# Performance work log

Hardware: AMD Instinct MI355X
Metric: run time of the kernel (lower is better)

Reference implementation:

```python
import jax, jax.numpy as jnp
import numpy as np

S, E, D, L, K = 32, 64, 256, 5, 5  # sentences, entities, feat dim, labels, support shots


def setup_inputs() -> dict:
    key = jax.random.key(0)
    k1, k2, k3, k4, k5, k6, k7 = jax.random.split(key, 7)
    scale = 1.0 / np.sqrt(D)
    return {
        "sup_entities": jax.random.normal(k1, (L, K, 2 * D), jnp.float32),
        "sup_context": jax.random.normal(k2, (L, K, D), jnp.float32),
        "x": jax.random.normal(k3, (S, E, D), jnp.float32),
        "context": jax.random.normal(k4, (S, E, E, D), jnp.float32),
        "W": jax.random.normal(k5, (D, D), jnp.float32) * scale,
        "Wself": jax.random.normal(k6, (D, D), jnp.float32) * scale,
        "counts": jax.random.randint(k7, (L,), 0, 9, jnp.int32),
    }


def reference(sup_entities, sup_context, x, context, W, Wself, counts):
    # per-label instance-count bias c_n = |n| / (total - |n|)
    cnt = counts.astype(jnp.float32) + 1.0
    total = jnp.sum(cnt)
    c = cnt / (total - cnt)  # [L]

    # prototypes (mean over support instances)
    proto = jnp.mean(sup_entities, axis=1)      # [L, 2D]
    ctx_center = jnp.mean(sup_context, axis=1)  # [L, D]

    # per-label edge weights: 1 / ||context[s,u,v] - ctx_center[k]||^2
    cn2 = jnp.sum(context * context, axis=-1)                        # [S,E,E]
    cc2 = jnp.sum(ctx_center * ctx_center, axis=-1)                  # [L]
    cross = jnp.einsum('suvd,kd->suvk', context, ctx_center)         # [S,E,E,L]
    d2 = cn2[..., None] - 2.0 * cross + cc2                          # [S,E,E,L]
    diag = jnp.eye(E, dtype=bool)
    w = jnp.where(diag[None, :, :, None], 0.0, 1.0 / jnp.maximum(d2, 1e-8))

    # GNN propagation per label: out[s,k,v] = x[s,v]@Wself + sum_u w[s,u,v,k] * (x[s,u]@W)
    xW = x @ W        # [S,E,D]
    xself = x @ Wself  # [S,E,D]
    out = xself[:, None, :, :] + jnp.einsum('suvk,sud->skvd', w, xW)  # [S,L,E,D]

    # squared distance of pred = cat(out[j], out[jp]) to each prototype n
    pa, pb = proto[:, :D], proto[:, D:]  # [L,D] each

    def sqd(o, p):  # o:[S,L,E,D], p:[L,D] -> [S,L,E,L]
        return (jnp.sum(o * o, axis=-1)[..., None]
                - 2.0 * jnp.einsum('skvd,nd->skvn', o, p)
                + jnp.sum(p * p, axis=-1))

    da = sqd(out, pa)  # [S,L,E,L]
    db = sqd(out, pb)  # [S,L,E,L]
    logits = da[:, :, :, None, :] + db[:, :, None, :, :] + c  # [S,L,E,E,L]
    pred = jax.nn.softmax(logits, axis=-1)
    # -> [sentence, entity_j, entity_j', weight_label_k, class_n]
    return jnp.transpose(pred, (0, 2, 3, 1, 4))
```

## Files before the change

### kernel.cpp

```cpp
#include <hip/hip_runtime.h>
#include <hip/hip_bf16.h>

#define SS 32
#define EE 64
#define DD 256
#define LL 5

typedef unsigned int uint32;

static __device__ __forceinline__ ushort f2bf(float f) {
    uint32 u = __float_as_uint(f);
    uint32 r = (u + 0x7FFFu + ((u >> 16) & 1u)) >> 16;
    return (ushort)r;
}
static __device__ __forceinline__ float bf2f(ushort h) {
    return __uint_as_float(((uint32)h) << 16);
}

template <int CTRL>
static __device__ __forceinline__ float dpp_add(float x) {
    int y = __builtin_amdgcn_update_dpp(0, __float_as_int(x), CTRL, 0xF, 0xF, true);
    return x + __int_as_float(y);
}
static __device__ __forceinline__ float red16(float x) {
    x = dpp_add<0xB1>(x);
    x = dpp_add<0x4E>(x);
    x = dpp_add<0x141>(x);
    x = dpp_add<0x140>(x);
    return x;
}


__global__ __launch_bounds__(256) void k0_setup(
    const float* __restrict__ sup_entities,
    const float* __restrict__ sup_context,
    const int*   __restrict__ counts,
    float* __restrict__ ws) {
    int b = blockIdx.x;
    int t = threadIdx.x, lane = t & 63, wv = t >> 6;
    __shared__ float part[4];

    if (b < 10) {
        int k = (b >= 5) ? b - 5 : b;
        int off = (b >= 5) ? 256 : 0;
        float s = 0.f;
#pragma unroll
        for (int j = 0; j < 5; j++) s += sup_entities[(k * 5 + j) * 512 + off + t];
        float m = s * 0.2f;
        ws[(b >= 5 ? 1280 : 0) + k * 256 + t] = m;
        float p = m * m;
#pragma unroll
        for (int o = 1; o < 64; o <<= 1) p += __shfl_xor(p, o);
        if (lane == 0) part[wv] = p;
        __syncthreads();
        if (t == 0) ws[2560 + b] = part[0] + part[1] + part[2] + part[3];
    } else {
        int k = b - 10;
        float s = 0.f;
#pragma unroll
        for (int j = 0; j < 5; j++) s += sup_context[(k * 5 + j) * DD + t];
        float m = s * 0.2f;
        ws[2576 + k * 256 + t] = m;
        float p = m * m;
#pragma unroll
        for (int o = 1; o < 64; o <<= 1) p += __shfl_xor(p, o);
        if (lane == 0) part[wv] = p;
        __syncthreads();
        if (t == 0) ws[3856 + k] = part[0] + part[1] + part[2] + part[3];
        if (b == 10 && t == 1) {
            float cnt[5], tot = 0.f;
#pragma unroll
            for (int q = 0; q < 5; q++) { cnt[q] = (float)counts[q] + 1.0f; tot += cnt[q]; }
#pragma unroll
            for (int q = 0; q < 5; q++) ws[2570 + q] = cnt[q] / (tot - cnt[q]);
        }
    }
}

__global__ __attribute__((amdgpu_waves_per_eu(2, 2))) __launch_bounds__(256)
void k1_gemm(
    const float* __restrict__ x, const float* __restrict__ W,
    const float* __restrict__ Wself, float* __restrict__ ws) {
    float* xself = ws + 4096;
    ushort* xw = (ushort*)(ws + 528384);

    int row0 = blockIdx.x * 8;
    int t = threadIdx.x, lane = t & 63, wv = t >> 6;

    float xreg[8];
    const float* xbase = x + row0 * DD + wv * 64 + lane;
#pragma unroll
    for (int r = 0; r < 8; r++) xreg[r] = xbase[r * DD];

    float4 accW[8], accS[8];
#pragma unroll
    for (int r = 0; r < 8; r++) {
        accW[r] = make_float4(0.f, 0.f, 0.f, 0.f);
        accS[r] = make_float4(0.f, 0.f, 0.f, 0.f);
    }
    const float4* Wp  = ((const float4*)W) + lane;
    const float4* Wsp = ((const float4*)Wself) + lane;
#pragma unroll 2
    for (int i = 0; i < 64; i++) {
        int kk = wv * 64 + i;
        float4 w4  = Wp[kk * 64];
        float4 ws4 = Wsp[kk * 64];
#pragma unroll
        for (int r = 0; r < 8; r++) {
            float xs = __uint_as_float(
                (uint32)__builtin_amdgcn_readlane((int)__float_as_uint(xreg[r]), i));
            accW[r].x = fmaf(xs, w4.x, accW[r].x);
            accW[r].y = fmaf(xs, w4.y, accW[r].y);
            accW[r].z = fmaf(xs, w4.z, accW[r].z);
            accW[r].w = fmaf(xs, w4.w, accW[r].w);
            accS[r].x = fmaf(xs, ws4.x, accS[r].x);
            accS[r].y = fmaf(xs, ws4.y, accS[r].y);
            accS[r].z = fmaf(xs, ws4.z, accS[r].z);
            accS[r].w = fmaf(xs, ws4.w, accS[r].w);
        }
    }
    __shared__ float4 redbuf[4][8][64];
#pragma unroll
    for (int r = 0; r < 8; r++) redbuf[wv][r][lane] = accS[r];
    __syncthreads();
    {
        int r = t >> 5;
#pragma unroll
        for (int f = 0; f < 2; f++) {
            int l4 = (t & 31) + 32 * f;
            float4 a = redbuf[0][r][l4], b = redbuf[1][r][l4];
            float4 c = redbuf[2][r][l4], d = redbuf[3][r][l4];
            float4 s4 = make_float4(a.x + b.x + c.x + d.x, a.y + b.y + c.y + d.y,
                                    a.z + b.z + c.z + d.z, a.w + b.w + c.w + d.w);
            *(float4*)&xself[(row0 + r) * DD + l4 * 4] = s4;
        }
    }
    __syncthreads();
#pragma unroll
    for (int r = 0; r < 8; r++) redbuf[wv][r][lane] = accW[r];
    __syncthreads();
    {
        int r = t >> 5;
#pragma unroll
        for (int f = 0; f < 2; f++) {
            int l4 = (t & 31) + 32 * f;
            float4 a = redbuf[0][r][l4], b = redbuf[1][r][l4];
            float4 c = redbuf[2][r][l4], d = redbuf[3][r][l4];
            float4 s4 = make_float4(a.x + b.x + c.x + d.x, a.y + b.y + c.y + d.y,
                                    a.z + b.z + c.z + d.z, a.w + b.w + c.w + d.w);
            ushort4 h;
            h.x = f2bf(s4.x); h.y = f2bf(s4.y); h.z = f2bf(s4.z); h.w = f2bf(s4.w);
            *(ushort4*)&xw[(row0 + r) * DD + l4 * 4] = h;
        }
    }
}

__global__ __attribute__((amdgpu_waves_per_eu(4, 4))) __launch_bounds__(256)
void k2_w(const float* __restrict__ context, float* __restrict__ ws) {
    float* wt = ws + 790528;

    int bx = blockIdx.x;
    int s = bx >> 6, u = bx & 63;
    int t = threadIdx.x, lane = t & 63, wv = t >> 6;
    int g = lane >> 4, gl = lane & 15;
    int G = wv * 4 + g;

    __shared__ float cc_l[1280];
    __shared__ float cc2_l[8];
    __shared__ float wbuf[5][64];

    for (int i = t; i < 320; i += 256)
        ((float4*)cc_l)[i] = ((const float4*)(ws + 2576))[i];
    if (t < 5) cc2_l[t] = ws[3856 + t];
    __syncthreads();

    float4 cc[5][4];
    float cc2r[5];
#pragma unroll
    for (int k = 0; k < 5; k++) {
#pragma unroll
        for (int j = 0; j < 4; j++)
            cc[k][j] = *(const float4*)&cc_l[k * 256 + j * 64 + gl * 4];
        cc2r[k] = cc2_l[k];
    }

    const float* base = context + (size_t)bx * (EE * DD) + gl * 4;
#pragma unroll
    for (int p = 0; p < 4; p++) {
        int v = p * 16 + G;
        const float* row = base + v * DD;
        float4 a[4];
#pragma unroll
        for (int j = 0; j < 4; j++) a[j] = *(const float4*)&row[j * 64];

        float cn = 0.f;
        float cr[5] = {0.f, 0.f, 0.f, 0.f, 0.f};
#pragma unroll
        for (int j = 0; j < 4; j++) {
            float4 c4 = a[j];
            cn = fmaf(c4.x, c4.x, fmaf(c4.y, c4.y, fmaf(c4.z, c4.z, fmaf(c4.w, c4.w, cn))));
#pragma unroll
            for (int k = 0; k < 5; k++) {
                float4 pp = cc[k][j];
                cr[k] = fmaf(c4.x, pp.x, fmaf(c4.y, pp.y, fmaf(c4.z, pp.z, fmaf(c4.w, pp.w, cr[k]))));
            }
        }
        cn = red16(cn);
#pragma unroll
        for (int k = 0; k < 5; k++) cr[k] = red16(cr[k]);
        if (gl == 0) {
#pragma unroll
            for (int k = 0; k < 5; k++) {
                float d2 = cn - 2.f * cr[k] + cc2r[k];
                wbuf[k][v] = (u == v) ? 0.f : 1.f / fmaxf(d2, 1e-8f);
            }
        }
    }
    __syncthreads();
    for (int i = t; i < 320; i += 256) {
        int k = i >> 6, v = i & 63;
        wt[(((size_t)s * 5 + k) * 64 + u) * 64 + v] = wbuf[k][v];
    }
}

__global__ __attribute__((amdgpu_waves_per_eu(2, 2))) __launch_bounds__(256)
void kB(const float* __restrict__ ws) {
    const ushort* xw = (const ushort*)(ws + 528384);
    const float* xself = ws + 4096;
    const float* wt = ws + 790528;
    float* da = (float*)(ws + 1445888);
    float* db = (float*)(ws + 1497088);

    int bx = blockIdx.x;
    int s = bx >> 4, vg = bx & 15;
    int t = threadIdx.x, lane = t & 63, wv = t >> 6;

    __shared__ ushort xw_l[64][256];
    __shared__ float  w_l[5][64][4];

    {
        const uint4* src = (const uint4*)(xw + (size_t)s * (EE * DD));
        uint4* dst = (uint4*)&xw_l[0][0];
#pragma unroll
        for (int j = 0; j < 8; j++) dst[j * 256 + t] = src[j * 256 + t];
    }
    for (int i = t; i < 320; i += 256) {
        int k = i >> 6, u = i & 63;
        *(float4*)&w_l[k][u][0] =
            *(const float4*)&wt[(((size_t)s * 5 + k) * 64 + u) * 64 + vg * 4];
    }
    __syncthreads();

    int v = vg * 4 + wv;
    float4 acc[5];
    {
        float4 xs = *(const float4*)&xself[((size_t)s * 64 + v) * DD + lane * 4];
#pragma unroll
        for (int k = 0; k < 5; k++) acc[k] = xs;
    }

#pragma unroll 4
    for (int u = 0; u < 64; u++) {
        ushort4 h4 = *(const ushort4*)&xw_l[u][lane * 4];
        float4 xv = make_float4(bf2f(h4.x), bf2f(h4.y), bf2f(h4.z), bf2f(h4.w));
#pragma unroll
        for (int k = 0; k < 5; k++) {
            float wk = w_l[k][u][wv];
            acc[k].x = fmaf(wk, xv.x, acc[k].x);
            acc[k].y = fmaf(wk, xv.y, acc[k].y);
            acc[k].z = fmaf(wk, xv.z, acc[k].z);
            acc[k].w = fmaf(wk, xv.w, acc[k].w);
        }
    }

    float4 pA[5], pB[5];
#pragma unroll
    for (int n = 0; n < 5; n++) {
        pA[n] = *(const float4*)&ws[n * 256 + lane * 4];
        pB[n] = *(const float4*)&ws[1280 + n * 256 + lane * 4];
    }
    float pa2r[5], pb2r[5];
#pragma unroll
    for (int n = 0; n < 5; n++) { pa2r[n] = ws[2560 + n]; pb2r[n] = ws[2565 + n]; }

#pragma unroll
    for (int k = 0; k < 5; k++) {
        float4 o = acc[k];
        float r[11];
        r[0] = fmaf(o.x, o.x, fmaf(o.y, o.y, fmaf(o.z, o.z, o.w * o.w)));
#pragma unroll
        for (int n = 0; n < 5; n++) {
            float4 p = pA[n];
            r[1 + n] = fmaf(o.x, p.x, fmaf(o.y, p.y, fmaf(o.z, p.z, o.w * p.w)));
            float4 q = pB[n];
            r[6 + n] = fmaf(o.x, q.x, fmaf(o.y, q.y, fmaf(o.z, q.z, o.w * q.w)));
        }
#pragma unroll
        for (int off = 1; off < 64; off <<= 1) {
#pragma unroll
            for (int q = 0; q < 11; q++) r[q] += __shfl_xor(r[q], off);
        }
        if (lane == 0) {
            size_t idx = (((size_t)s * 5 + k) * 64 + v) * 5;
#pragma unroll
            for (int n = 0; n < 5; n++) {
                da[idx + n] = r[0] - 2.f * r[1 + n] + pa2r[n];
                db[idx + n] = r[0] - 2.f * r[6 + n] + pb2r[n];
            }
        }
    }
}

__global__ __launch_bounds__(320) void kC(const float* __restrict__ ws,
                                          float* __restrict__ out) {
    const float* da = ws + 1445888;
    const float* db = ws + 1497088;
    int bx = blockIdx.x;
    int s = bx >> 6, v1 = bx & 63;
    int t = threadIdx.x;
    int v2 = t / 5, k = t - v2 * 5;

    __shared__ float ob[1600];
    __shared__ float cvs[5];
    if (t < 5) cvs[t] = ws[2570 + t];

    const float* dap = da + (((size_t)s * 5 + k) * 64 + v1) * 5;
    const float* dbp = db + (((size_t)s * 5 + k) * 64 + v2) * 5;
    float l0[5];
#pragma unroll
    for (int n = 0; n < 5; n++) l0[n] = dap[n] + dbp[n];
    __syncthreads();
    float m = -3.4e38f;
#pragma unroll
    for (int n = 0; n < 5; n++) { l0[n] += cvs[n]; m = fmaxf(m, l0[n]); }
    float e[5], sum = 0.f;
#pragma unroll
    for (int n = 0; n < 5; n++) { e[n] = __expf(l0[n] - m); sum += e[n]; }
    float r = 1.f / sum;
#pragma unroll
    for (int n = 0; n < 5; n++) ob[t * 5 + n] = e[n] * r;
    __syncthreads();

    const float4* ob4 = (const float4*)ob;
    float4* op = (float4*)(out + (size_t)bx * 1600);
    for (int i = t; i < 400; i += 320) op[i] = ob4[i];
}

extern "C" void kernel_launch(void* const* d_in, const int* in_sizes, int n_in,
                              void* d_out, int out_size, void* d_ws, size_t ws_size,
                              hipStream_t stream) {
    const float* sup_entities = (const float*)d_in[0];
    const float* sup_context  = (const float*)d_in[1];
    const float* x            = (const float*)d_in[2];
    const float* context      = (const float*)d_in[3];
    const float* W            = (const float*)d_in[4];
    const float* Wself        = (const float*)d_in[5];
    const int*   counts       = (const int*)d_in[6];
    float* out = (float*)d_out;
    float* ws = (float*)d_ws;

    k0_setup<<<15, 256, 0, stream>>>(sup_entities, sup_context, counts, ws);
    k2_w<<<SS * EE, 256, 0, stream>>>(context, ws);
    k1_gemm<<<256, 256, 0, stream>>>(x, W, Wself, ws);
    kB<<<512, 256, 0, stream>>>(ws);
    kC<<<SS * EE, 320, 0, stream>>>(ws, out);
}
```

Measured before the change: 73.09 us.

## Fuse setup into weight kernel and use readlane broadcasts in propagation

Folds the prototype/context-center setup kernel into the edge-weight kernel, so each weight block recomputes the context centers and their norms from the support context, and 10 extra blocks handle the entity prototypes and count bias. This removes one kernel launch and its dependency. In the propagation kernel, edge weights are loaded per lane into registers and broadcast with readlane instead of staged through shared memory, and the loop is fully unrolled. The 64-lane reductions switch from shuffle-xor to DPP row ops plus readlane. The cost is redundant per-block recomputation of the centers and larger unrolled code.

```diff
diff --git a/kernel.cpp b/kernel.cpp
--- a/kernel.cpp
+++ b/kernel.cpp
@@ -29,18 +29,28 @@
     x = dpp_add<0x140>(x);
     return x;
 }
-
-
-__global__ __launch_bounds__(256) void k0_setup(
-    const float* __restrict__ sup_entities,
-    const float* __restrict__ sup_context,
-    const int*   __restrict__ counts,
-    float* __restrict__ ws) {
-    int b = blockIdx.x;
+static __device__ __forceinline__ float red64_scalar(float x) {
+    x = red16(x);
+    x = dpp_add<0x142>(x);
+    x = dpp_add<0x143>(x);
+    return __uint_as_float((uint32)__builtin_amdgcn_readlane(__float_as_int(x), 63));
+}
+
+
+__global__ __attribute__((amdgpu_waves_per_eu(4, 4))) __launch_bounds__(256)
+void k2f(const float* __restrict__ context, const float* __restrict__ sup_context,
+         const float* __restrict__ sup_entities, const int* __restrict__ counts,
+         float* __restrict__ ws) {
+    int bx = blockIdx.x;
     int t = threadIdx.x, lane = t & 63, wv = t >> 6;
+
+    __shared__ float cc_l[1280];
+    __shared__ float cc2_l[8];
+    __shared__ float wbuf[5][64];
     __shared__ float part[4];
 
-    if (b < 10) {
+    if (bx >= 2048) {
+        int b = bx - 2048;
         int k = (b >= 5) ? b - 5 : b;
         int off = (b >= 5) ? 256 : 0;
         float s = 0.f;
@@ -54,26 +64,86 @@
         if (lane == 0) part[wv] = p;
         __syncthreads();
         if (t == 0) ws[2560 + b] = part[0] + part[1] + part[2] + part[3];
-    } else {
-        int k = b - 10;
-        float s = 0.f;
-#pragma unroll
-        for (int j = 0; j < 5; j++) s += sup_context[(k * 5 + j) * DD + t];
-        float m = s * 0.2f;
-        ws[2576 + k * 256 + t] = m;
-        float p = m * m;
-#pragma unroll
-        for (int o = 1; o < 64; o <<= 1) p += __shfl_xor(p, o);
-        if (lane == 0) part[wv] = p;
-        __syncthreads();
-        if (t == 0) ws[3856 + k] = part[0] + part[1] + part[2] + part[3];
-        if (b == 10 && t == 1) {
+        if (b == 0 && t == 1) {
             float cnt[5], tot = 0.f;
 #pragma unroll
             for (int q = 0; q < 5; q++) { cnt[q] = (float)counts[q] + 1.0f; tot += cnt[q]; }
 #pragma unroll
             for (int q = 0; q < 5; q++) ws[2570 + q] = cnt[q] / (tot - cnt[q]);
         }
+        return;
+    }
+
+    int s = bx >> 6, u = bx & 63;
+    int g = lane >> 4, gl = lane & 15;
+    int G = wv * 4 + g;
+
+    for (int i = t; i < 1280; i += 256) {
+        int k = i >> 8, d = i & 255;
+        float sum = 0.f;
+#pragma unroll
+        for (int j = 0; j < 5; j++) sum += sup_context[(k * 5 + j) * DD + d];
+        cc_l[i] = sum * 0.2f;
+    }
+    __syncthreads();
+    if (t < 80) {
+        int k = t >> 4, gg = t & 15;
+        float p = 0.f;
+#pragma unroll
+        for (int j = 0; j < 16; j++) { float v = cc_l[k * 256 + gg * 16 + j]; p = fmaf(v, v, p); }
+#pragma unroll
+        for (int o = 1; o < 16; o <<= 1) p += __shfl_xor(p, o);
+        if (gg == 0) cc2_l[k] = p;
+    }
+    __syncthreads();
+
+    float4 cc[5][4];
+    float cc2r[5];
+#pragma unroll
+    for (int k = 0; k < 5; k++) {
+#pragma unroll
+        for (int j = 0; j < 4; j++)
+            cc[k][j] = *(const float4*)&cc_l[k * 256 + j * 64 + gl * 4];
+        cc2r[k] = cc2_l[k];
+    }
+
+    float* wt = ws + 790528;
+    const float* base = context + (size_t)bx * (EE * DD) + gl * 4;
+#pragma unroll
+    for (int p = 0; p < 4; p++) {
+        int v = p * 16 + G;
+        const float* row = base + v * DD;
+        float4 a[4];
+#pragma unroll
+        for (int j = 0; j < 4; j++) a[j] = *(const float4*)&row[j * 64];
+
+        float cn = 0.f;
+        float cr[5] = {0.f, 0.f, 0.f, 0.f, 0.f};
+#pragma unroll
+        for (int j = 0; j < 4; j++) {
+            float4 c4 = a[j];
+            cn = fmaf(c4.x, c4.x, fmaf(c4.y, c4.y, fmaf(c4.z, c4.z, fmaf(c4.w, c4.w, cn))));
+#pragma unroll
+            for (int k = 0; k < 5; k++) {
+                float4 pp = cc[k][j];
+                cr[k] = fmaf(c4.x, pp.x, fmaf(c4.y, pp.y, fmaf(c4.z, pp.z, fmaf(c4.w, pp.w, cr[k]))));
+            }
+        }
+        cn = red16(cn);
+#pragma unroll
+        for (int k = 0; k < 5; k++) cr[k] = red16(cr[k]);
+        if (gl == 0) {
+#pragma unroll
+            for (int k = 0; k < 5; k++) {
+                float d2 = cn - 2.f * cr[k] + cc2r[k];
+                wbuf[k][v] = (u == v) ? 0.f : 1.f / fmaxf(d2, 1e-8f);
+            }
+        }
+    }
+    __syncthreads();
+    for (int i = t; i < 320; i += 256) {
+        int k = i >> 6, v = i & 63;
+        wt[(((size_t)s * 5 + k) * 64 + u) * 64 + v] = wbuf[k][v];
     }
 }
 
@@ -155,74 +225,6 @@
     }
 }
 
-__global__ __attribute__((amdgpu_waves_per_eu(4, 4))) __launch_bounds__(256)
-void k2_w(const float* __restrict__ context, float* __restrict__ ws) {
-    float* wt = ws + 790528;
-
-    int bx = blockIdx.x;
-    int s = bx >> 6, u = bx & 63;
-    int t = threadIdx.x, lane = t & 63, wv = t >> 6;
-    int g = lane >> 4, gl = lane & 15;
-    int G = wv * 4 + g;
-
-    __shared__ float cc_l[1280];
-    __shared__ float cc2_l[8];
-    __shared__ float wbuf[5][64];
-
-    for (int i = t; i < 320; i += 256)
-        ((float4*)cc_l)[i] = ((const float4*)(ws + 2576))[i];
-    if (t < 5) cc2_l[t] = ws[3856 + t];
-    __syncthreads();
-
-    float4 cc[5][4];
-    float cc2r[5];
-#pragma unroll
-    for (int k = 0; k < 5; k++) {
-#pragma unroll
-        for (int j = 0; j < 4; j++)
-            cc[k][j] = *(const float4*)&cc_l[k * 256 + j * 64 + gl * 4];
-        cc2r[k] = cc2_l[k];
-    }
-
-    const float* base = context + (size_t)bx * (EE * DD) + gl * 4;
-#pragma unroll
-    for (int p = 0; p < 4; p++) {
-        int v = p * 16 + G;
-        const float* row = base + v * DD;
-        float4 a[4];
-#pragma unroll
-        for (int j = 0; j < 4; j++) a[j] = *(const float4*)&row[j * 64];
-
-        float cn = 0.f;
-        float cr[5] = {0.f, 0.f, 0.f, 0.f, 0.f};
-#pragma unroll
-        for (int j = 0; j < 4; j++) {
-            float4 c4 = a[j];
-            cn = fmaf(c4.x, c4.x, fmaf(c4.y, c4.y, fmaf(c4.z, c4.z, fmaf(c4.w, c4.w, cn))));
-#pragma unroll
-            for (int k = 0; k < 5; k++) {
-                float4 pp = cc[k][j];
-                cr[k] = fmaf(c4.x, pp.x, fmaf(c4.y, pp.y, fmaf(c4.z, pp.z, fmaf(c4.w, pp.w, cr[k]))));
-            }
-        }
-        cn = red16(cn);
-#pragma unroll
-        for (int k = 0; k < 5; k++) cr[k] = red16(cr[k]);
-        if (gl == 0) {
-#pragma unroll
-            for (int k = 0; k < 5; k++) {
-                float d2 = cn - 2.f * cr[k] + cc2r[k];
-                wbuf[k][v] = (u == v) ? 0.f : 1.f / fmaxf(d2, 1e-8f);
-            }
-        }
-    }
-    __syncthreads();
-    for (int i = t; i < 320; i += 256) {
-        int k = i >> 6, v = i & 63;
-        wt[(((size_t)s * 5 + k) * 64 + u) * 64 + v] = wbuf[k][v];
-    }
-}
-
 __global__ __attribute__((amdgpu_waves_per_eu(2, 2))) __launch_bounds__(256)
 void kB(const float* __restrict__ ws) {
     const ushort* xw = (const ushort*)(ws + 528384);
@@ -234,9 +236,14 @@
     int bx = blockIdx.x;
     int s = bx >> 4, vg = bx & 15;
     int t = threadIdx.x, lane = t & 63, wv = t >> 6;
+    int v = vg * 4 + wv;
 
     __shared__ ushort xw_l[64][256];
-    __shared__ float  w_l[5][64][4];
+
+    float wreg[5];
+#pragma unroll
+    for (int k = 0; k < 5; k++)
+        wreg[k] = wt[(((size_t)s * 5 + k) * 64 + lane) * 64 + v];
 
     {
         const uint4* src = (const uint4*)(xw + (size_t)s * (EE * DD));
@@ -244,28 +251,23 @@
 #pragma unroll
         for (int j = 0; j < 8; j++) dst[j * 256 + t] = src[j * 256 + t];
     }
-    for (int i = t; i < 320; i += 256) {
-        int k = i >> 6, u = i & 63;
-        *(float4*)&w_l[k][u][0] =
-            *(const float4*)&wt[(((size_t)s * 5 + k) * 64 + u) * 64 + vg * 4];
-    }
-    __syncthreads();
-
-    int v = vg * 4 + wv;
+
     float4 acc[5];
     {
         float4 xs = *(const float4*)&xself[((size_t)s * 64 + v) * DD + lane * 4];
 #pragma unroll
         for (int k = 0; k < 5; k++) acc[k] = xs;
     }
-
-#pragma unroll 4
+    __syncthreads();
+
+#pragma unroll
     for (int u = 0; u < 64; u++) {
         ushort4 h4 = *(const ushort4*)&xw_l[u][lane * 4];
         float4 xv = make_float4(bf2f(h4.x), bf2f(h4.y), bf2f(h4.z), bf2f(h4.w));
 #pragma unroll
         for (int k = 0; k < 5; k++) {
-            float wk = w_l[k][u][wv];
+            float wk = __uint_as_float(
+                (uint32)__builtin_amdgcn_readlane(__float_as_int(wreg[k]), u));
             acc[k].x = fmaf(wk, xv.x, acc[k].x);
             acc[k].y = fmaf(wk, xv.y, acc[k].y);
             acc[k].z = fmaf(wk, xv.z, acc[k].z);
@@ -295,17 +297,15 @@
             float4 q = pB[n];
             r[6 + n] = fmaf(o.x, q.x, fmaf(o.y, q.y, fmaf(o.z, q.z, o.w * q.w)));
         }
-#pragma unroll
-        for (int off = 1; off < 64; off <<= 1) {
-#pragma unroll
-            for (int q = 0; q < 11; q++) r[q] += __shfl_xor(r[q], off);
-        }
+        float tot[11];
+#pragma unroll
+        for (int q = 0; q < 11; q++) tot[q] = red64_scalar(r[q]);
         if (lane == 0) {
             size_t idx = (((size_t)s * 5 + k) * 64 + v) * 5;
 #pragma unroll
             for (int n = 0; n < 5; n++) {
-                da[idx + n] = r[0] - 2.f * r[1 + n] + pa2r[n];
-                db[idx + n] = r[0] - 2.f * r[6 + n] + pb2r[n];
+                da[idx + n] = tot[0] - 2.f * tot[1 + n] + pa2r[n];
+                db[idx + n] = tot[0] - 2.f * tot[6 + n] + pb2r[n];
             }
         }
     }
@@ -359,8 +359,7 @@
     float* out = (float*)d_out;
     float* ws = (float*)d_ws;
 
-    k0_setup<<<15, 256, 0, stream>>>(sup_entities, sup_context, counts, ws);
-    k2_w<<<SS * EE, 256, 0, stream>>>(context, ws);
+    k2f<<<SS * EE + 10, 256, 0, stream>>>(context, sup_context, sup_entities, counts, ws);
     k1_gemm<<<256, 256, 0, stream>>>(x, W, Wself, ws);
     kB<<<512, 256, 0, stream>>>(ws);
     kC<<<SS * EE, 320, 0, stream>>>(ws, out);
```

New measurement: 117.2 us. +60.4%, slower.
